# Kernel tuning notes

Hardware: AMD Instinct MI355X
Metric: run time of the kernel (lower is better)

Reference implementation:

```python
import jax, jax.numpy as jnp
import numpy as np

EPS = 1e-5
D = 32          # token embedding dim
HEADS = 8
DH = D // HEADS  # 4


def _layernorm(x, g, b):
    mu = jnp.mean(x, axis=-1, keepdims=True)
    var = jnp.mean(jnp.square(x - mu), axis=-1, keepdims=True)
    return (x - mu) / jnp.sqrt(var + EPS) * g + b


def _mhsa(x, Wqvk, W0):
    # x: [..., t, 32]; Wqvk: [96, 32]; W0: [32, 32]
    qkv = x @ Wqvk.T                                   # [..., t, 96]
    qkv = qkv.reshape(qkv.shape[:-1] + (DH, 3, HEADS))  # (d k h) layout of original rearrange
    q, k, v = qkv[..., 0, :], qkv[..., 1, :], qkv[..., 2, :]  # [..., t, d, h]
    scores = jnp.einsum('...tdh,...sdh->...hts', q, k) * (DH ** -0.5)
    attn = jax.nn.softmax(scores, axis=-1)
    out = jnp.einsum('...hts,...sdh->...thd', attn, v)  # [..., t, h, d]
    out = out.reshape(out.shape[:-2] + (D,))            # (h d) concat order
    return out @ W0.T


def setup_inputs() -> dict:
    key = jax.random.key(0)
    ks = jax.random.split(key, 8)
    B = 256
    s = D ** -0.5
    return {
        'x':       jax.random.normal(ks[0], (B, 3, 32, 32, 32), dtype=jnp.float32),
        'pos_y':   jax.random.normal(ks[1], (3, 32, 32), dtype=jnp.float32) * s,
        'Wqvk_y':  jax.random.normal(ks[2], (3, 3 * D, D), dtype=jnp.float32) * s,
        'W0_y':    jax.random.normal(ks[3], (3, D, D), dtype=jnp.float32) * s,
        'g_y':     jnp.ones((D,), dtype=jnp.float32),
        'b_y':     jnp.zeros((D,), dtype=jnp.float32),
        'Wqvk_x':  jax.random.normal(ks[4], (3, 3 * D, D), dtype=jnp.float32) * s,
        'W0_x':    jax.random.normal(ks[5], (3, D, D), dtype=jnp.float32) * s,
        'g_x':     jnp.ones((D,), dtype=jnp.float32),
        'b_x':     jnp.zeros((D,), dtype=jnp.float32),
    }


def reference(x, pos_y, Wqvk_y, W0_y, g_y, b_y, Wqvk_x, W0_x, g_x, b_x):
    # x: [b, 3, l, w, h] with l=w=h=32. Dropout layers are in eval mode (identity).
    tst = jnp.transpose(x, (0, 1, 4, 2, 3))               # [b, 3, i(=h), t(=l), d(=w)]
    # AbsPosEmb1D per RGB channel: in_ @ pos^T
    emb = jnp.einsum('bcitd,cjd->bcitj', tst, pos_y)      # [b, 3, 32, 32, 32]
    outs = []
    for c in range(3):  # distinct r/g/b weights
        o = _mhsa(emb[:, c], Wqvk_y[c], W0_y[c])
        outs.append(_layernorm(emb[:, c] + o, g_y, b_y))
    x_tmp = jnp.stack(outs, axis=1)                       # [b, 3, i, t, 32]
    x_tmp = jnp.transpose(x_tmp, (0, 1, 3, 4, 2))         # [b, 3, t, 32, i]
    x1 = jax.nn.sigmoid(x_tmp) * x                        # first gating

    # BUG in original second loop: it reuses the stale `emb_y` from the last
    # iteration of the first loop (channel b, i = width-1) for every (i, j).
    emb_last = emb[:, 2, -1]                              # [b, 32, 32]
    ys = []
    for c in range(3):
        o = _mhsa(emb_last, Wqvk_x[c], W0_x[c])
        ys.append(_layernorm(emb_last + o, g_x, b_x))
    tmp2 = jnp.stack(ys, axis=1)                          # [b, 3, t, 32]
    # y stacked over i (constant across i), then permuted to [b,3,32,i,32]
    y_perm = jnp.transpose(tmp2, (0, 1, 3, 2))[:, :, :, None, :]  # [b,3,32,1,32]
    return jax.nn.sigmoid(y_perm) * x1
```

## Files before the change

### kernel.cpp

```cpp
#include <hip/hip_runtime.h>
#include <hip/hip_bf16.h>


using bf16 = __hip_bfloat16;
typedef float v2f __attribute__((ext_vector_type(2)));
using short8 = __attribute__((ext_vector_type(8))) short;
using f32x4  = __attribute__((ext_vector_type(4))) float;

__device__ __forceinline__ v2f pk_fma(v2f acc, v2f a, v2f b) {
  asm("v_pk_fma_f32 %0, %1, %2, %0" : "+v"(acc) : "v"(a), "v"(b));
  return acc;
}

template <int CTRL>
__device__ __forceinline__ float dpp_add(float x) {
  return x + __int_as_float(
      __builtin_amdgcn_mov_dpp(__float_as_int(x), CTRL, 0xF, 0xF, true));
}

__device__ __forceinline__ ushort bf16_rne(float f) {
  uint u = __float_as_uint(f);
  return (ushort)((u + 0x7FFFu + ((u >> 16) & 1u)) >> 16);
}
__device__ __forceinline__ void split2(float x, ushort& h, ushort& l) {
  h = bf16_rne(x);
  l = bf16_rne(x - __uint_as_float((uint)h << 16));
}

struct __align__(16) SMem {
  ushort xsH[32][40];
  ushort xsL[32][40];
  union {
    struct { ushort WH[128][40]; ushort WL[128][40]; } w;
    struct {
      float esT[32][40];
      float aoF[32][36];
      float w0s[32][36];
    } s;
  } u;
  float qS[32][36];
  float kT[32][36];
  float vT[32][36];
};

__global__ __launch_bounds__(256) void wc_kernel(
    const float* __restrict__ pos_y, const float* __restrict__ wqvk_y,
    const float* __restrict__ wqvk_x, ushort* __restrict__ wc2)
{
  const int n6 = blockIdx.x;
  const int c = n6 % 3, xset = n6 / 3;
  const float* W = (xset ? wqvk_x : wqvk_y) + c * 3072;
  const float* P = pos_y + (xset ? 2 : c) * 1024;
  __shared__ float Ws[96][33];
  __shared__ float Ps[32][33];
  const int tid = threadIdx.x;
#pragma unroll
  for (int k = 0; k < 12; ++k) {
    const int e = tid * 12 + k;
    Ws[e >> 5][e & 31] = W[e];
  }
#pragma unroll
  for (int k = 0; k < 4; ++k) {
    const int e = tid * 4 + k;
    Ps[e >> 5][e & 31] = P[e];
  }
  __syncthreads();
  const int n = tid & 127, half = tid >> 7;
  float src[16];
  if (n >= 96) {
    const int j = n - 96;
#pragma unroll
    for (int dd = 0; dd < 16; ++dd) src[dd] = Ps[j][16 * half + dd];
  } else {
    const int sidx = n >> 5;
    const int m = n & 31, dh = m & 3, h = m >> 2;
    const int f = dh * 24 + (sidx == 0 ? 8 : (sidx == 1 ? 16 : 0)) + h;
    const float sc = (sidx == 2) ? 0.72134752f : 1.0f;
#pragma unroll
    for (int dd = 0; dd < 16; ++dd) {
      float s = 0.f;
      for (int j = 0; j < 32; ++j) s += Ws[f][j] * Ps[j][16 * half + dd];
      src[dd] = s * sc;
    }
  }
  ushort* base = wc2 + (size_t)n6 * 8192;
#pragma unroll
  for (int dd = 0; dd < 16; ++dd) {
    ushort h, l;
    split2(src[dd], h, l);
    base[n * 32 + 16 * half + dd]        = h;
    base[4096 + n * 32 + 16 * half + dd] = l;
  }
}

__device__ __forceinline__ void load_tables(
    SMem& sm, int tid, const float* __restrict__ xbc, int i,
    const ushort* __restrict__ wc2,
    const float* __restrict__ g, const float* __restrict__ b)
{
  const int t = tid >> 3, dq = (tid & 7) * 4;
  float xv[4];
#pragma unroll
  for (int k = 0; k < 4; ++k) xv[k] = xbc[(t * 32 + dq + k) * 32 + i];
  ushort hs[4], ls[4];
#pragma unroll
  for (int k = 0; k < 4; ++k) split2(xv[k], hs[k], ls[k]);
  *(short4*)&sm.xsH[t][dq] = make_short4((short)hs[0], (short)hs[1],
                                         (short)hs[2], (short)hs[3]);
  *(short4*)&sm.xsL[t][dq] = make_short4((short)ls[0], (short)ls[1],
                                         (short)ls[2], (short)ls[3]);
  {
    const float4* src = (const float4*)(wc2 + tid * 32);
    float4 r0 = src[0], r1 = src[1], r2 = src[2], r3 = src[3];
    ushort* dst = (tid < 128) ? &sm.u.w.WH[tid][0] : &sm.u.w.WL[tid - 128][0];
    ((float4*)dst)[0] = r0; ((float4*)dst)[1] = r1;
    ((float4*)dst)[2] = r2; ((float4*)dst)[3] = r3;
  }
  if (tid < 32) {
    sm.qS[tid][32] = g[tid] * 1.44269504f;
    sm.qS[tid][33] = b[tid] * 1.44269504f;
  }
}

__device__ __forceinline__ void mhsa_core(SMem& sm, int tid,
                                          const float* __restrict__ w0g,
                                          float sig_out[2][2])
{
  const int wv = tid >> 6, lane = tid & 63;
  const int lr = lane & 15, lk = lane >> 4;
  const int mt = wv >> 1;
  const int qe = wv & 1;
  const int t0 = mt * 16 + lk * 4;
  f32x4 eC0 = {0.f,0.f,0.f,0.f}, eC1 = {0.f,0.f,0.f,0.f};

  {
    short8 aH = *(const short8*)&sm.xsH[mt * 16 + lr][lk * 8];
    short8 aL = *(const short8*)&sm.xsL[mt * 16 + lr][lk * 8];
    f32x4 acc[4];
#pragma unroll
    for (int q = 0; q < 4; ++q) {
      const int n = qe * 64 + q * 16 + lr;
      short8 bH = *(const short8*)&sm.u.w.WH[n][lk * 8];
      short8 bL = *(const short8*)&sm.u.w.WL[n][lk * 8];
      f32x4 c = {0.f, 0.f, 0.f, 0.f};
      c = __builtin_amdgcn_mfma_f32_16x16x32_bf16(aH, bH, c, 0, 0, 0);
      c = __builtin_amdgcn_mfma_f32_16x16x32_bf16(aH, bL, c, 0, 0, 0);
      c = __builtin_amdgcn_mfma_f32_16x16x32_bf16(aL, bH, c, 0, 0, 0);
      acc[q] = c;
    }
    if (qe == 0) {
      *(f32x4*)&sm.kT[lr][t0]      = acc[0];
      *(f32x4*)&sm.kT[lr + 16][t0] = acc[1];
      *(f32x4*)&sm.vT[lr][t0]      = acc[2];
      *(f32x4*)&sm.vT[lr + 16][t0] = acc[3];
    } else {
#pragma unroll
      for (int r = 0; r < 4; ++r) {
        sm.qS[t0 + r][lr]      = acc[0][r];
        sm.qS[t0 + r][lr + 16] = acc[1][r];
      }
      eC0 = acc[2]; eC1 = acc[3];
    }
  }
  float4 w0v = *(const float4*)&w0g[tid * 4];
  __syncthreads();
  if (qe == 1) {
    *(f32x4*)&sm.u.s.esT[lr][t0]      = eC0;
    *(f32x4*)&sm.u.s.esT[lr + 16][t0] = eC1;
  }
  { const int e = tid * 4; *(float4*)&sm.u.s.w0s[e >> 5][e & 31] = w0v; }

  {
    const int h = tid >> 5, tg2 = (tid >> 2) & 7, sg2 = tid & 3;
    const int ta = 4 * tg2, s0 = 8 * sg2;
    float4 qr0 = *(const float4*)&sm.qS[ta + 0][4 * h];
    float4 qr1 = *(const float4*)&sm.qS[ta + 1][4 * h];
    float4 qr2 = *(const float4*)&sm.qS[ta + 2][4 * h];
    float4 qr3 = *(const float4*)&sm.qS[ta + 3][4 * h];
    const float qa_[4][4] = {
        {qr0.x, qr0.y, qr0.z, qr0.w},
        {qr1.x, qr1.y, qr1.z, qr1.w},
        {qr2.x, qr2.y, qr2.z, qr2.w},
        {qr3.x, qr3.y, qr3.z, qr3.w}};
    v2f sc[4][4];
#pragma unroll
    for (int kk = 0; kk < 4; ++kk)
#pragma unroll
      for (int sp2 = 0; sp2 < 4; ++sp2) sc[kk][sp2] = v2f{0.f, 0.f};
#pragma unroll
    for (int dh = 0; dh < 4; ++dh) {
      const float* kr = &sm.kT[4 * h + dh][s0];
      float4 ka = *(const float4*)&kr[0];
      float4 kb = *(const float4*)&kr[4];
      v2f k0{ka.x, ka.y}, k1{ka.z, ka.w}, k2{kb.x, kb.y}, k3{kb.z, kb.w};
#pragma unroll
      for (int kk = 0; kk < 4; ++kk) {
        v2f qv{qa_[kk][dh], qa_[kk][dh]};
        sc[kk][0] = pk_fma(sc[kk][0], qv, k0);
        sc[kk][1] = pk_fma(sc[kk][1], qv, k1);
        sc[kk][2] = pk_fma(sc[kk][2], qv, k2);
        sc[kk][3] = pk_fma(sc[kk][3], qv, k3);
      }
    }
    float inv[4];
#pragma unroll
    for (int kk = 0; kk < 4; ++kk) {
#pragma unroll
      for (int sp2 = 0; sp2 < 4; ++sp2) {
        sc[kk][sp2][0] = exp2f(sc[kk][sp2][0]);
        sc[kk][sp2][1] = exp2f(sc[kk][sp2][1]);
      }
      v2f dv = sc[kk][0] + sc[kk][1];
      v2f dw = sc[kk][2] + sc[kk][3];
      dv += dw;
      float dn = dv[0] + dv[1];
      dn = dpp_add<0xB1>(dn);
      dn = dpp_add<0x4E>(dn);
      inv[kk] = __fdividef(1.0f, dn);
    }
    v2f pv[4][4];
#pragma unroll
    for (int kk = 0; kk < 4; ++kk)
#pragma unroll
      for (int dh = 0; dh < 4; ++dh) pv[kk][dh] = v2f{0.f, 0.f};
#pragma unroll
    for (int dh = 0; dh < 4; ++dh) {
      const float* vr = &sm.vT[4 * h + dh][s0];
      float4 va = *(const float4*)&vr[0];
      float4 vb = *(const float4*)&vr[4];
      v2f v0{va.x, va.y}, v1{va.z, va.w}, v2v{vb.x, vb.y}, v3{vb.z, vb.w};
#pragma unroll
      for (int kk = 0; kk < 4; ++kk) {
        pv[kk][dh] = pk_fma(pv[kk][dh], sc[kk][0], v0);
        pv[kk][dh] = pk_fma(pv[kk][dh], sc[kk][1], v1);
        pv[kk][dh] = pk_fma(pv[kk][dh], sc[kk][2], v2v);
        pv[kk][dh] = pk_fma(pv[kk][dh], sc[kk][3], v3);
      }
    }
    float ov[4][4];
#pragma unroll
    for (int kk = 0; kk < 4; ++kk)
#pragma unroll
      for (int dh = 0; dh < 4; ++dh) {
        float o = pv[kk][dh][0] + pv[kk][dh][1];
        o = dpp_add<0xB1>(o);
        o = dpp_add<0x4E>(o);
        ov[kk][dh] = o;
      }
    if (sg2 == 0) {
#pragma unroll
      for (int kk = 0; kk < 4; ++kk) {
        *(float4*)&sm.u.s.aoF[ta + kk][4 * h] = make_float4(
            ov[kk][0] * inv[kk], ov[kk][1] * inv[kk],
            ov[kk][2] * inv[kk], ov[kk][3] * inv[kk]);
      }
    }
  }
  __syncthreads();

  {
    const int g = tid >> 4, l = tid & 15;
    v2f a00{0.f,0.f}, a01{0.f,0.f}, a10{0.f,0.f}, a11{0.f,0.f};
#pragma unroll
    for (int f4 = 0; f4 < 8; ++f4) {
      float4 u0 = *(const float4*)&sm.u.s.aoF[g][4 * f4];
      float4 u1 = *(const float4*)&sm.u.s.aoF[g + 16][4 * f4];
      float4 w0 = *(const float4*)&sm.u.s.w0s[l][4 * f4];
      float4 w1 = *(const float4*)&sm.u.s.w0s[l + 16][4 * f4];
      a00 = pk_fma(a00, v2f{u0.x, u0.y}, v2f{w0.x, w0.y});
      a00 = pk_fma(a00, v2f{u0.z, u0.w}, v2f{w0.z, w0.w});
      a01 = pk_fma(a01, v2f{u0.x, u0.y}, v2f{w1.x, w1.y});
      a01 = pk_fma(a01, v2f{u0.z, u0.w}, v2f{w1.z, w1.w});
      a10 = pk_fma(a10, v2f{u1.x, u1.y}, v2f{w0.x, w0.y});
      a10 = pk_fma(a10, v2f{u1.z, u1.w}, v2f{w0.z, w0.w});
      a11 = pk_fma(a11, v2f{u1.x, u1.y}, v2f{w1.x, w1.y});
      a11 = pk_fma(a11, v2f{u1.z, u1.w}, v2f{w1.z, w1.w});
    }
    float rr[2][2];
    rr[0][0] = a00[0] + a00[1] + sm.u.s.esT[l][g];
    rr[0][1] = a01[0] + a01[1] + sm.u.s.esT[l + 16][g];
    rr[1][0] = a10[0] + a10[1] + sm.u.s.esT[l][g + 16];
    rr[1][1] = a11[0] + a11[1] + sm.u.s.esT[l + 16][g + 16];
    float s1a = rr[0][0] + rr[0][1], s1b = rr[1][0] + rr[1][1];
    float s2a = rr[0][0]*rr[0][0] + rr[0][1]*rr[0][1];
    float s2b = rr[1][0]*rr[1][0] + rr[1][1]*rr[1][1];
    s1a = dpp_add<0xB1>(s1a); s1a = dpp_add<0x4E>(s1a);
    s1a = dpp_add<0x124>(s1a); s1a = dpp_add<0x128>(s1a);
    s2a = dpp_add<0xB1>(s2a); s2a = dpp_add<0x4E>(s2a);
    s2a = dpp_add<0x124>(s2a); s2a = dpp_add<0x128>(s2a);
    s1b = dpp_add<0xB1>(s1b); s1b = dpp_add<0x4E>(s1b);
    s1b = dpp_add<0x124>(s1b); s1b = dpp_add<0x128>(s1b);
    s2b = dpp_add<0xB1>(s2b); s2b = dpp_add<0x4E>(s2b);
    s2b = dpp_add<0x124>(s2b); s2b = dpp_add<0x128>(s2b);
    const float mua = s1a * (1.0f / 32.0f), mub = s1b * (1.0f / 32.0f);
    const float ra = rsqrtf(s2a * (1.0f / 32.0f) - mua * mua + 1e-5f);
    const float rb = rsqrtf(s2b * (1.0f / 32.0f) - mub * mub + 1e-5f);
    const float g0 = sm.qS[l][32],      b0 = sm.qS[l][33];
    const float g1 = sm.qS[l + 16][32], b1 = sm.qS[l + 16][33];
    sig_out[0][0] = __fdividef(1.0f, 1.0f + exp2f(-((rr[0][0] - mua) * ra * g0 + b0)));
    sig_out[0][1] = __fdividef(1.0f, 1.0f + exp2f(-((rr[0][1] - mua) * ra * g1 + b1)));
    sig_out[1][0] = __fdividef(1.0f, 1.0f + exp2f(-((rr[1][0] - mub) * rb * g0 + b0)));
    sig_out[1][1] = __fdividef(1.0f, 1.0f + exp2f(-((rr[1][1] - mub) * rb * g1 + b1)));
  }
}

__global__ __launch_bounds__(256, 4) void phase1_kernel(
    const float* __restrict__ x, const ushort* __restrict__ wc2,
    const float* __restrict__ w0_x,
    const float* __restrict__ g_x, const float* __restrict__ b_x,
    bf16* __restrict__ gates)
{
  __shared__ SMem sm;
  const int tid = threadIdx.x;
  const int n = blockIdx.x;
  const int c = n % 3, b = n / 3;
  const float* xbc = x + (size_t)(b * 3 + 2) * 32768;
  load_tables(sm, tid, xbc, 31, wc2 + (size_t)(3 + c) * 8192, g_x, b_x);
  __syncthreads();
  float sig[2][2];
  mhsa_core(sm, tid, w0_x + c * 1024, sig);
  const int g = tid >> 4, l = tid & 15;
#pragma unroll
  for (int u = 0; u < 2; ++u)
#pragma unroll
    for (int v = 0; v < 2; ++v)
      gates[((c * 256 + b) * 32 + g + 16 * u) * 32 + l + 16 * v] =
          __float2bfloat16(sig[u][v]);
}

__global__ __launch_bounds__(256, 4) void phase2_kernel(
    const float* __restrict__ x, const ushort* __restrict__ wc2,
    const float* __restrict__ w0_y,
    const float* __restrict__ g_y, const float* __restrict__ b_y,
    const bf16* __restrict__ gates, float* __restrict__ out)
{
  __shared__ SMem sm;
  const int tid = threadIdx.x;
  const int n = blockIdx.x;
  const int p = (n & 7) * 3072 + (n >> 3);
  const int i = p & 31, bc = p >> 5;
  const int c = bc % 3, b = bc / 3;
  const float* xbc = x + (size_t)bc * 32768;
  load_tables(sm, tid, xbc, i, wc2 + (size_t)c * 8192, g_y, b_y);
  if (tid < 32)
    sm.kT[tid][32] = __bfloat162float(gates[((c * 256 + b) * 32 + i) * 32 + tid]);
  __syncthreads();
  float sig[2][2];
  mhsa_core(sm, tid, w0_y + c * 1024, sig);
  const int g = tid >> 4, l = tid & 15;
  float* ob = out + (size_t)bc * 32768 + i;
#pragma unroll
  for (int u = 0; u < 2; ++u) {
    const int r = g + 16 * u;
    const float sgv = sm.kT[r][32];
#pragma unroll
    for (int v = 0; v < 2; ++v) {
      const int cc = l + 16 * v;
      const float xv = __uint_as_float((uint)sm.xsH[r][cc] << 16) +
                       __uint_as_float((uint)sm.xsL[r][cc] << 16);
      ob[(r * 32 + cc) * 32] = sgv * sig[u][v] * xv;
    }
  }
}

extern "C" void kernel_launch(void* const* d_in, const int* in_sizes, int n_in,
                              void* d_out, int out_size, void* d_ws, size_t ws_size,
                              hipStream_t stream) {
  const float* x      = (const float*)d_in[0];
  const float* pos_y  = (const float*)d_in[1];
  const float* wqvk_y = (const float*)d_in[2];
  const float* w0_y   = (const float*)d_in[3];
  const float* g_y    = (const float*)d_in[4];
  const float* b_y    = (const float*)d_in[5];
  const float* wqvk_x = (const float*)d_in[6];
  const float* w0_x   = (const float*)d_in[7];
  const float* g_x    = (const float*)d_in[8];
  const float* b_x    = (const float*)d_in[9];
  bf16*   gates = (bf16*)d_ws;
  ushort* wc2   = (ushort*)((char*)d_ws + 1572864);

  hipLaunchKernelGGL(wc_kernel, dim3(6), dim3(256), 0, stream,
                     pos_y, wqvk_y, wqvk_x, wc2);
  hipLaunchKernelGGL(phase1_kernel, dim3(768), dim3(256), 0, stream,
                     x, wc2, w0_x, g_x, b_x, gates);
  hipLaunchKernelGGL(phase2_kernel, dim3(24576), dim3(256), 0, stream,
                     x, wc2, w0_y, g_y, b_y, gates, (float*)d_out);
}
```

Baseline: 400.8 us.

## Pre-swizzle MFMA fragments and XOR-swizzle q/k/v LDS to shrink shared memory

Weights and x tiles are now stored in MFMA fragment order, so each lane reads a contiguous short8. The padded q/k/v tables become unpadded XOR-swizzled 32x32 arrays, and the esT padding drops from 40 to 36. LayerNorm gamma/beta and the gate values now live in registers instead of LDS. The smaller LDS footprint lets launch bounds rise to 5 blocks per CU, which aims at higher occupancy and fewer bank conflicts. The risk is more register pressure and possible spills.

```diff
diff --git a/kernel.cpp b/kernel.cpp
--- a/kernel.cpp
+++ b/kernel.cpp
@@ -27,21 +27,40 @@
   l = bf16_rne(x - __uint_as_float((uint)h << 16));
 }
 
+__device__ __forceinline__ int frag_idx(int row, int k) {
+  return ((row >> 4) << 9) + (((row & 15) + ((k >> 3) << 4)) << 3) + (k & 7);
+}
+
 struct __align__(16) SMem {
-  ushort xsH[32][40];
-  ushort xsL[32][40];
+  ushort xsH[1024];
+  ushort xsL[1024];
   union {
-    struct { ushort WH[128][40]; ushort WL[128][40]; } w;
+    ushort W[8192];
     struct {
-      float esT[32][40];
+      float esT[32][36];
       float aoF[32][36];
       float w0s[32][36];
     } s;
   } u;
-  float qS[32][36];
-  float kT[32][36];
-  float vT[32][36];
+  float qS[1024];
+  float kT[1024];
+  float vT[1024];
 };
+
+__device__ __forceinline__ float* swz_q(float* base, int t, int c) {
+  return (float*)((char*)base + (((t << 7) + (c << 2)) ^ (((t >> 1) & 7) << 4)));
+}
+__device__ __forceinline__ const float* swz_qc(const float* base, int t, int c) {
+  return (const float*)((const char*)base +
+                        (((t << 7) + (c << 2)) ^ (((t >> 1) & 7) << 4)));
+}
+__device__ __forceinline__ float* swz_kv(float* base, int r, int s) {
+  return (float*)((char*)base + (((r << 7) + (s << 2)) ^ ((r & 7) << 4)));
+}
+__device__ __forceinline__ const float* swz_kvc(const float* base, int r, int s) {
+  return (const float*)((const char*)base +
+                        (((r << 7) + (s << 2)) ^ ((r & 7) << 4)));
+}
 
 __global__ __launch_bounds__(256) void wc_kernel(
     const float* __restrict__ pos_y, const float* __restrict__ wqvk_y,
@@ -84,19 +103,21 @@
     }
   }
   ushort* base = wc2 + (size_t)n6 * 8192;
+  const int tile = n >> 4, rr = n & 15;
 #pragma unroll
   for (int dd = 0; dd < 16; ++dd) {
-    ushort h, l;
-    split2(src[dd], h, l);
-    base[n * 32 + 16 * half + dd]        = h;
-    base[4096 + n * 32 + 16 * half + dd] = l;
+    const int k = 16 * half + dd;
+    const int off = tile * 512 + ((rr + ((k >> 3) << 4)) << 3) + (k & 7);
+    ushort hh, ll;
+    split2(src[dd], hh, ll);
+    base[off]        = hh;
+    base[4096 + off] = ll;
   }
 }
 
 __device__ __forceinline__ void load_tables(
     SMem& sm, int tid, const float* __restrict__ xbc, int i,
-    const ushort* __restrict__ wc2,
-    const float* __restrict__ g, const float* __restrict__ b)
+    const ushort* __restrict__ wc2)
 {
   const int t = tid >> 3, dq = (tid & 7) * 4;
   float xv[4];
@@ -105,25 +126,22 @@
   ushort hs[4], ls[4];
 #pragma unroll
   for (int k = 0; k < 4; ++k) split2(xv[k], hs[k], ls[k]);
-  *(short4*)&sm.xsH[t][dq] = make_short4((short)hs[0], (short)hs[1],
-                                         (short)hs[2], (short)hs[3]);
-  *(short4*)&sm.xsL[t][dq] = make_short4((short)ls[0], (short)ls[1],
-                                         (short)ls[2], (short)ls[3]);
+  const int off = frag_idx(t, dq);
+  *(short4*)&sm.xsH[off] = make_short4((short)hs[0], (short)hs[1],
+                                       (short)hs[2], (short)hs[3]);
+  *(short4*)&sm.xsL[off] = make_short4((short)ls[0], (short)ls[1],
+                                       (short)ls[2], (short)ls[3]);
   {
     const float4* src = (const float4*)(wc2 + tid * 32);
     float4 r0 = src[0], r1 = src[1], r2 = src[2], r3 = src[3];
-    ushort* dst = (tid < 128) ? &sm.u.w.WH[tid][0] : &sm.u.w.WL[tid - 128][0];
-    ((float4*)dst)[0] = r0; ((float4*)dst)[1] = r1;
-    ((float4*)dst)[2] = r2; ((float4*)dst)[3] = r3;
-  }
-  if (tid < 32) {
-    sm.qS[tid][32] = g[tid] * 1.44269504f;
-    sm.qS[tid][33] = b[tid] * 1.44269504f;
+    float4* dst = (float4*)(sm.u.W + tid * 32);
+    dst[0] = r0; dst[1] = r1; dst[2] = r2; dst[3] = r3;
   }
 }
 
 __device__ __forceinline__ void mhsa_core(SMem& sm, int tid,
                                           const float* __restrict__ w0g,
+                                          float g0, float b0, float g1, float b1,
                                           float sig_out[2][2])
 {
   const int wv = tid >> 6, lane = tid & 63;
@@ -134,14 +152,14 @@
   f32x4 eC0 = {0.f,0.f,0.f,0.f}, eC1 = {0.f,0.f,0.f,0.f};
 
   {
-    short8 aH = *(const short8*)&sm.xsH[mt * 16 + lr][lk * 8];
-    short8 aL = *(const short8*)&sm.xsL[mt * 16 + lr][lk * 8];
+    short8 aH = *(const short8*)&sm.xsH[mt * 512 + lane * 8];
+    short8 aL = *(const short8*)&sm.xsL[mt * 512 + lane * 8];
     f32x4 acc[4];
 #pragma unroll
     for (int q = 0; q < 4; ++q) {
-      const int n = qe * 64 + q * 16 + lr;
-      short8 bH = *(const short8*)&sm.u.w.WH[n][lk * 8];
-      short8 bL = *(const short8*)&sm.u.w.WL[n][lk * 8];
+      const int tile = qe * 4 + q;
+      short8 bH = *(const short8*)&sm.u.W[tile * 512 + lane * 8];
+      short8 bL = *(const short8*)&sm.u.W[4096 + tile * 512 + lane * 8];
       f32x4 c = {0.f, 0.f, 0.f, 0.f};
       c = __builtin_amdgcn_mfma_f32_16x16x32_bf16(aH, bH, c, 0, 0, 0);
       c = __builtin_amdgcn_mfma_f32_16x16x32_bf16(aH, bL, c, 0, 0, 0);
@@ -149,15 +167,15 @@
       acc[q] = c;
     }
     if (qe == 0) {
-      *(f32x4*)&sm.kT[lr][t0]      = acc[0];
-      *(f32x4*)&sm.kT[lr + 16][t0] = acc[1];
-      *(f32x4*)&sm.vT[lr][t0]      = acc[2];
-      *(f32x4*)&sm.vT[lr + 16][t0] = acc[3];
+      *(f32x4*)swz_kv(sm.kT, lr,      t0) = acc[0];
+      *(f32x4*)swz_kv(sm.kT, lr + 16, t0) = acc[1];
+      *(f32x4*)swz_kv(sm.vT, lr,      t0) = acc[2];
+      *(f32x4*)swz_kv(sm.vT, lr + 16, t0) = acc[3];
     } else {
 #pragma unroll
       for (int r = 0; r < 4; ++r) {
-        sm.qS[t0 + r][lr]      = acc[0][r];
-        sm.qS[t0 + r][lr + 16] = acc[1][r];
+        *swz_q(sm.qS, t0 + r, lr)      = acc[0][r];
+        *swz_q(sm.qS, t0 + r, lr + 16) = acc[1][r];
       }
       eC0 = acc[2]; eC1 = acc[3];
     }
@@ -173,10 +191,10 @@
   {
     const int h = tid >> 5, tg2 = (tid >> 2) & 7, sg2 = tid & 3;
     const int ta = 4 * tg2, s0 = 8 * sg2;
-    float4 qr0 = *(const float4*)&sm.qS[ta + 0][4 * h];
-    float4 qr1 = *(const float4*)&sm.qS[ta + 1][4 * h];
-    float4 qr2 = *(const float4*)&sm.qS[ta + 2][4 * h];
-    float4 qr3 = *(const float4*)&sm.qS[ta + 3][4 * h];
+    float4 qr0 = *(const float4*)swz_qc(sm.qS, ta + 0, 4 * h);
+    float4 qr1 = *(const float4*)swz_qc(sm.qS, ta + 1, 4 * h);
+    float4 qr2 = *(const float4*)swz_qc(sm.qS, ta + 2, 4 * h);
+    float4 qr3 = *(const float4*)swz_qc(sm.qS, ta + 3, 4 * h);
     const float qa_[4][4] = {
         {qr0.x, qr0.y, qr0.z, qr0.w},
         {qr1.x, qr1.y, qr1.z, qr1.w},
@@ -189,9 +207,8 @@
       for (int sp2 = 0; sp2 < 4; ++sp2) sc[kk][sp2] = v2f{0.f, 0.f};
 #pragma unroll
     for (int dh = 0; dh < 4; ++dh) {
-      const float* kr = &sm.kT[4 * h + dh][s0];
-      float4 ka = *(const float4*)&kr[0];
-      float4 kb = *(const float4*)&kr[4];
+      float4 ka = *(const float4*)swz_kvc(sm.kT, 4 * h + dh, s0);
+      float4 kb = *(const float4*)swz_kvc(sm.kT, 4 * h + dh, s0 + 4);
       v2f k0{ka.x, ka.y}, k1{ka.z, ka.w}, k2{kb.x, kb.y}, k3{kb.z, kb.w};
 #pragma unroll
       for (int kk = 0; kk < 4; ++kk) {
@@ -225,9 +242,8 @@
       for (int dh = 0; dh < 4; ++dh) pv[kk][dh] = v2f{0.f, 0.f};
 #pragma unroll
     for (int dh = 0; dh < 4; ++dh) {
-      const float* vr = &sm.vT[4 * h + dh][s0];
-      float4 va = *(const float4*)&vr[0];
-      float4 vb = *(const float4*)&vr[4];
+      float4 va = *(const float4*)swz_kvc(sm.vT, 4 * h + dh, s0);
+      float4 vb = *(const float4*)swz_kvc(sm.vT, 4 * h + dh, s0 + 4);
       v2f v0{va.x, va.y}, v1{va.z, va.w}, v2v{vb.x, vb.y}, v3{vb.z, vb.w};
 #pragma unroll
       for (int kk = 0; kk < 4; ++kk) {
@@ -295,8 +311,6 @@
     const float mua = s1a * (1.0f / 32.0f), mub = s1b * (1.0f / 32.0f);
     const float ra = rsqrtf(s2a * (1.0f / 32.0f) - mua * mua + 1e-5f);
     const float rb = rsqrtf(s2b * (1.0f / 32.0f) - mub * mub + 1e-5f);
-    const float g0 = sm.qS[l][32],      b0 = sm.qS[l][33];
-    const float g1 = sm.qS[l + 16][32], b1 = sm.qS[l + 16][33];
     sig_out[0][0] = __fdividef(1.0f, 1.0f + exp2f(-((rr[0][0] - mua) * ra * g0 + b0)));
     sig_out[0][1] = __fdividef(1.0f, 1.0f + exp2f(-((rr[0][1] - mua) * ra * g1 + b1)));
     sig_out[1][0] = __fdividef(1.0f, 1.0f + exp2f(-((rr[1][0] - mub) * rb * g0 + b0)));
@@ -304,7 +318,7 @@
   }
 }
 
-__global__ __launch_bounds__(256, 4) void phase1_kernel(
+__global__ __launch_bounds__(256, 5) void phase1_kernel(
     const float* __restrict__ x, const ushort* __restrict__ wc2,
     const float* __restrict__ w0_x,
     const float* __restrict__ g_x, const float* __restrict__ b_x,
@@ -314,12 +328,16 @@
   const int tid = threadIdx.x;
   const int n = blockIdx.x;
   const int c = n % 3, b = n / 3;
+  const int l = tid & 15;
+  const float L2E = 1.44269504f;
+  const float g0 = g_x[l] * L2E,      b0 = b_x[l] * L2E;
+  const float g1 = g_x[l + 16] * L2E, b1 = b_x[l + 16] * L2E;
   const float* xbc = x + (size_t)(b * 3 + 2) * 32768;
-  load_tables(sm, tid, xbc, 31, wc2 + (size_t)(3 + c) * 8192, g_x, b_x);
+  load_tables(sm, tid, xbc, 31, wc2 + (size_t)(3 + c) * 8192);
   __syncthreads();
   float sig[2][2];
-  mhsa_core(sm, tid, w0_x + c * 1024, sig);
-  const int g = tid >> 4, l = tid & 15;
+  mhsa_core(sm, tid, w0_x + c * 1024, g0, b0, g1, b1, sig);
+  const int g = tid >> 4;
 #pragma unroll
   for (int u = 0; u < 2; ++u)
 #pragma unroll
@@ -328,7 +346,7 @@
           __float2bfloat16(sig[u][v]);
 }
 
-__global__ __launch_bounds__(256, 4) void phase2_kernel(
+__global__ __launch_bounds__(256, 5) void phase2_kernel(
     const float* __restrict__ x, const ushort* __restrict__ wc2,
     const float* __restrict__ w0_y,
     const float* __restrict__ g_y, const float* __restrict__ b_y,
@@ -340,25 +358,30 @@
   const int p = (n & 7) * 3072 + (n >> 3);
   const int i = p & 31, bc = p >> 5;
   const int c = bc % 3, b = bc / 3;
+  const int g = tid >> 4, l = tid & 15;
+  const float L2E = 1.44269504f;
+  const float g0 = g_y[l] * L2E,      b0 = b_y[l] * L2E;
+  const float g1 = g_y[l + 16] * L2E, b1 = b_y[l + 16] * L2E;
+  const int gbase = ((c * 256 + b) * 32 + i) * 32;
+  const float sg0 = __bfloat162float(gates[gbase + g]);
+  const float sg1 = __bfloat162float(gates[gbase + g + 16]);
   const float* xbc = x + (size_t)bc * 32768;
-  load_tables(sm, tid, xbc, i, wc2 + (size_t)c * 8192, g_y, b_y);
-  if (tid < 32)
-    sm.kT[tid][32] = __bfloat162float(gates[((c * 256 + b) * 32 + i) * 32 + tid]);
+  load_tables(sm, tid, xbc, i, wc2 + (size_t)c * 8192);
   __syncthreads();
   float sig[2][2];
-  mhsa_core(sm, tid, w0_y + c * 1024, sig);
-  const int g = tid >> 4, l = tid & 15;
+  mhsa_core(sm, tid, w0_y + c * 1024, g0, b0, g1, b1, sig);
   float* ob = out + (size_t)bc * 32768 + i;
 #pragma unroll
   for (int u = 0; u < 2; ++u) {
     const int r = g + 16 * u;
-    const float sgv = sm.kT[r][32];
+    const float sgv = (u == 0) ? sg0 : sg1;
 #pragma unroll
     for (int v = 0; v < 2; ++v) {
       const int cc = l + 16 * v;
-      const float xv = __uint_as_float((uint)sm.xsH[r][cc] << 16) +
-                       __uint_as_float((uint)sm.xsL[r][cc] << 16);
-      ob[(r * 32 + cc) * 32] = sgv * sig[u][v] * xv;
+      const int off = frag_idx(r, cc);
+      const float xvv = __uint_as_float((uint)sm.xsH[off] << 16) +
+                        __uint_as_float((uint)sm.xsL[off] << 16);
+      ob[(r * 32 + cc) * 32] = sgv * sig[u][v] * xvv;
     }
   }
 }
```

New measurement: 455.5 us. 1.14x slower.
